# Kernel tuning notes

Measured on AMD Instinct MI355X. Metric: run time of the kernel, lower is better.

## Reference

```python
import jax, jax.numpy as jnp
import numpy as np

N_NODES = 50000
N_EDGES = 1_600_000
F_IN = 128
F_OUT = 8
K_TAPS = 4
AVG_DEG = 32.0


def setup_inputs() -> dict:
    key = jax.random.key(0)
    k1, k2, k3, k4, k5 = jax.random.split(key, 5)
    x = jax.random.normal(k1, (N_NODES, F_IN), dtype=jnp.float32)
    gso_rows = jax.random.randint(k2, (N_EDGES,), 0, N_NODES, dtype=jnp.int32)
    gso_cols = jax.random.randint(k3, (N_EDGES,), 0, N_NODES, dtype=jnp.int32)
    gso_vals = jax.random.uniform(k4, (N_EDGES,), dtype=jnp.float32) / AVG_DEG
    # filterCoeff = randn(outFeat, filter_order) * 0.1 as in torch __init__
    coeff = jax.random.normal(k5, (F_OUT, K_TAPS), dtype=jnp.float32) * 0.1
    return {"x": x, "gso_rows": gso_rows, "gso_cols": gso_cols,
            "gso_vals": gso_vals, "coeff": coeff}


def reference(x, gso_rows, gso_cols, gso_vals, coeff):
    # Faithful to the torch code INCLUDING its carried-over SpMV state:
    # output feature o uses powers S^{1+o(K-1)} .. S^{o(K-1)+K} of x.
    F_out, K = coeff.shape
    N = x.shape[0]
    max_power = F_out * (K - 1) + 1  # highest S power needed

    def spmv(Z):  # S @ Z via edge-list gather + segment_sum scatter
        return jax.ops.segment_sum(gso_vals[:, None] * Z[gso_cols], gso_rows,
                                   num_segments=N)

    def step(Z, _):
        Zn = spmv(Z)
        return Zn, Zn.sum(axis=1)  # sum over in-features done up-front

    # s[p-1, n] = sum_f (S^p x)[n, f], for p = 1..max_power
    _, s = jax.lax.scan(step, x, None, length=max_power)  # (max_power, N)

    # power index (0-based into s) used by output o, tap i: o*(K-1) + i
    idx = jnp.arange(F_out)[:, None] * (K - 1) + jnp.arange(K)[None, :]  # (F_out, K)
    sg = s[idx]  # (F_out, K, N)
    y = jnp.einsum('ok,okn->no', coeff, sg)  # (N, F_out)
    return y
```

## Files before the change

### kernel.cpp

```cpp
#include <hip/hip_runtime.h>
#include <hip/hip_bf16.h>

#define N_NODES 50000
#define NPAD    50176
#define N_EDGES 1600000
#define F_IN    128
#define F_OUT   8
#define K_TAPS  4
#define MAX_POWER 25

#define NBLK    256
#define NTHR    512
#define RPB     196
#define CHUNK   6272
#define NPART   256
#define NTHR_P  512
#define ECAP_G  8192
#define ECAP_L  7168
#define NITER   14
#define CSB     800

typedef int v4i __attribute__((ext_vector_type(4)));

__device__ inline int wave_incl_scan(int v, int lane) {
    #pragma unroll
    for (int off = 1; off < 64; off <<= 1) {
        int t = __shfl_up(v, off, 64);
        if (lane >= off) v += t;
    }
    return v;
}

__device__ inline void st_coh_i(int* p, int v) {
    __hip_atomic_store(p, v, __ATOMIC_RELAXED, __HIP_MEMORY_SCOPE_AGENT);
}
__device__ inline void st_coh_i4(v4i* p, v4i v) {
    asm volatile("global_store_dwordx4 %0, %1, off sc0 sc1"
                 :: "v"(p), "v"(v) : "memory");
}
__device__ inline v4i ld_coh_i4(const v4i* p) {
    v4i v;
    asm volatile("global_load_dwordx4 %0, %1, off sc0 sc1\n\t"
                 "s_waitcnt vmcnt(0)"
                 : "=&v"(v) : "v"(p) : "memory");
    return v;
}

__global__ void rowsum_kernel(const float* __restrict__ x,
                              float* __restrict__ u, int n_nodes) {
    int tid = threadIdx.x;
    int lane = tid & 63;
    int wid = tid >> 6;
    int half = lane >> 5;
    int l = lane & 31;
    int node = blockIdx.x * 8 + wid * 2 + half;
    if (node >= n_nodes) return;
    float4 v = ((const float4*)(x + (size_t)node * F_IN))[l];
    float s = v.x + v.y + v.z + v.w;
    #pragma unroll
    for (int off = 16; off > 0; off >>= 1)
        s += __shfl_down(s, off, 32);
    if (l == 0) u[node] = s;
}

__global__ void partition_kernel(const int* __restrict__ rows,
                                 const int* __restrict__ cols,
                                 const float* __restrict__ vals,
                                 int* __restrict__ gcnt,
                                 int2* __restrict__ edges, int n_edges) {
    __shared__ int lhist[NBLK];
    __shared__ int lcur[NBLK];
    __shared__ int lbase[NBLK];
    __shared__ int2 stage[CHUNK];
    __shared__ unsigned char sbkt[CHUNK];
    __shared__ int wsum[4];
    int tid = threadIdx.x;
    int base = blockIdx.x * CHUNK;
    int cend = min(base + CHUNK, n_edges);

    if (tid < NBLK) lhist[tid] = 0;
    __syncthreads();
    for (int i = base + tid; i < cend; i += NTHR_P)
        atomicAdd(&lhist[rows[i] / RPB], 1);
    __syncthreads();

    int lane = tid & 63, wid = tid >> 6;
    int h = 0, incl = 0;
    if (tid < NBLK) {
        h = lhist[tid];
        incl = wave_incl_scan(h, lane);
        if (lane == 63) wsum[wid] = incl;
    }
    __syncthreads();
    if (tid < NBLK) {
        int woff = 0;
        for (int w = 0; w < wid; ++w) woff += wsum[w];
        int excl = woff + incl - h;
        lcur[tid] = excl;
        if (h) {
            int g = atomicAdd(&gcnt[tid], h);
            lbase[tid] = tid * ECAP_G + g - excl;
        }
    }
    __syncthreads();

    for (int i = base + tid; i < cend; i += NTHR_P) {
        int r = rows[i], c = cols[i];
        float v = vals[i];
        int b = r / RPB;
        int pos = atomicAdd(&lcur[b], 1);
        stage[pos] = make_int2(((r - b * RPB) << 16) | c, __float_as_int(v));
        sbkt[pos] = (unsigned char)b;
    }
    __syncthreads();

    int cn = cend - base;
    for (int i = tid; i < cn; i += NTHR_P) {
        int b = sbkt[i];
        int o = lbase[b] + i;
        if (o - b * ECAP_G < ECAP_G)
            edges[o] = stage[i];
    }
}

__global__ __launch_bounds__(NTHR, 1)
void chain_kernel(const int* __restrict__ gcnt,
                  const int2* __restrict__ edges,
                  const float* __restrict__ coeff,
                  const float* __restrict__ u,
                  float* __restrict__ s,
                  float* __restrict__ y,
                  int* __restrict__ flags,
                  int n_nodes) {
    __shared__ int2  esort[ECAP_L];
    __shared__ int   chist[CSB];
    __shared__ int   ccur[CSB];
    __shared__ int   wsum8[8];
    __shared__ __align__(16) float acc[RPB];
    __shared__ float yacc[RPB * F_OUT];
    __shared__ float lcoeff[F_OUT * K_TAPS];

    int tid = threadIdx.x;
    int b = blockIdx.x;

    if (tid < RPB) acc[tid] = 0.f;
    for (int j = tid; j < RPB * F_OUT; j += NTHR) yacc[j] = 0.f;
    if (tid < F_OUT * K_TAPS) lcoeff[tid] = coeff[tid];

    int cnt = min(gcnt[b], ECAP_G);
    const int2* eb = edges + (size_t)b * ECAP_G;

    for (int i = tid; i < CSB; i += NTHR) chist[i] = 0;
    __syncthreads();
    if (cnt <= ECAP_L) {
        for (int i = tid; i < cnt; i += NTHR) {
            int2 e = eb[i];
            atomicAdd(&chist[(e.x & 0xFFFF) >> 6], 1);
        }
        __syncthreads();
        int lane = tid & 63, wid = tid >> 6;
        int b0 = 2 * tid;
        int h0 = (b0 < CSB) ? chist[b0] : 0;
        int h1 = (b0 + 1 < CSB) ? chist[b0 + 1] : 0;
        int ps = h0 + h1;
        int incl = wave_incl_scan(ps, lane);
        if (lane == 63) wsum8[wid] = incl;
        __syncthreads();
        int woff = 0;
        for (int w = 0; w < wid; ++w) woff += wsum8[w];
        int ex = woff + incl - ps;
        if (b0 < CSB) ccur[b0] = ex;
        if (b0 + 1 < CSB) ccur[b0 + 1] = ex + h0;
        __syncthreads();
        for (int i = tid; i < cnt; i += NTHR) {
            int2 e = eb[i];
            int pos = atomicAdd(&ccur[(e.x & 0xFFFF) >> 6], 1);
            esort[pos] = e;
        }
        __syncthreads();
    } else {
        int cl = min(cnt, ECAP_L);
        for (int i = tid; i < cl; i += NTHR) esort[i] = eb[i];
        __syncthreads();
    }

    int   ecol[NITER];
    int   erow[NITER];
    float eval[NITER];
    int cntl = min(cnt, ECAP_L);
    #pragma unroll
    for (int j = 0; j < NITER; ++j) {
        int idx = tid + j * NTHR;
        int2 e = (idx < cntl) ? esort[idx] : make_int2(0, 0);
        ecol[j] = e.x & 0xFFFF;
        erow[j] = e.x >> 16;
        eval[j] = __int_as_float(e.y);
    }

    for (int p = 0; p < MAX_POWER; ++p) {
        const float* __restrict__ src = (p == 0) ? u : s + (size_t)(p - 1) * NPAD;
        float* dst = s + (size_t)p * NPAD;

        float v[NITER];
        #pragma unroll
        for (int j = 0; j < NITER; ++j) v[j] = src[ecol[j]];
        #pragma unroll
        for (int j = 0; j < NITER; ++j)
            if (tid + j * NTHR < cntl)
                atomicAdd(&acc[erow[j]], eval[j] * v[j]);
        for (int k = ECAP_L + tid; k < cnt; k += NTHR) {
            int2 ev = eb[k];
            atomicAdd(&acc[ev.x >> 16], __int_as_float(ev.y) * src[ev.x & 0xFFFF]);
        }
        __syncthreads();

        float val = (tid < RPB) ? acc[tid] : 0.f;
        bool last = (p == MAX_POWER - 1);

        if (!last && tid < RPB / 4) {
            v4i av = ((const v4i*)acc)[tid];
            st_coh_i4(((v4i*)(dst + (size_t)b * RPB)) + tid, av);
        }

        if (tid < RPB) {
            #pragma unroll
            for (int o = 0; o < F_OUT; ++o) {
                int k = p - (K_TAPS - 1) * o;
                if (k >= 0 && k < K_TAPS)
                    yacc[tid * F_OUT + o] += lcoeff[o * K_TAPS + k] * val;
            }
        }

        if (!last) {
            if (tid == 0) {
                asm volatile("s_waitcnt vmcnt(0)" ::: "memory");
                st_coh_i(&flags[b], p + 1);
            }
            __syncthreads();
            if (tid < RPB) acc[tid] = 0.f;
            if (tid < NBLK / 4) {
                const v4i* fp = ((const v4i*)flags) + tid;
                int target = p + 1;
                while (true) {
                    v4i f = ld_coh_i4(fp);
                    int m = min(min(f[0], f[1]), min(f[2], f[3]));
                    if (__all(m >= target)) break;
                    __builtin_amdgcn_s_sleep(1);
                }
            }
            __syncthreads();
        }
    }

    __syncthreads();
    for (int j = tid; j < RPB * F_OUT; j += NTHR) {
        int row = b * RPB + (j >> 3);
        if (row < n_nodes) y[(size_t)row * F_OUT + (j & 7)] = yacc[j];
    }
}

extern "C" void kernel_launch(void* const* d_in, const int* in_sizes, int n_in,
                              void* d_out, int out_size, void* d_ws, size_t ws_size,
                              hipStream_t stream) {
    const float* x        = (const float*)d_in[0];
    const int*   gso_rows = (const int*)d_in[1];
    const int*   gso_cols = (const int*)d_in[2];
    const float* gso_vals = (const float*)d_in[3];
    const float* coeff    = (const float*)d_in[4];
    float* y = (float*)d_out;

    float* u     = (float*)d_ws;
    float* s     = u + NPAD;
    int2*  edges = (int2*)(s + (size_t)MAX_POWER * NPAD);
    int*   gcnt  = (int*)(edges + (size_t)NBLK * ECAP_G);
    int*   flags = gcnt + NBLK;

    (void)hipMemsetAsync(gcnt, 0, (size_t)(NBLK + NBLK) * sizeof(int), stream);

    partition_kernel<<<NPART, NTHR_P, 0, stream>>>(
        gso_rows, gso_cols, gso_vals, gcnt, edges, N_EDGES);

    rowsum_kernel<<<(N_NODES + 7) / 8, 256, 0, stream>>>(x, u, N_NODES);

    int n_nodes = N_NODES;
    void* args[] = { (void*)&gcnt, (void*)&edges, (void*)&coeff,
                     (void*)&u, (void*)&s, (void*)&y, (void*)&flags,
                     (void*)&n_nodes };
    (void)hipLaunchCooperativeKernel((void*)chain_kernel, dim3(NBLK), dim3(NTHR),
                                     args, 0, stream);
}
```

Before: 475.8 us.

## Replace grid-wide flag barrier with per-element sentinel polling dataflow

Removes the per-power grid barrier built on a flags array. Instead, every power buffer is pre-filled with a NaN sentinel and consumers poll each gathered value until it is no longer the sentinel. The accumulator is double-buffered so the block needs only one __syncthreads per power. The goal is to let blocks proceed as soon as their actual dependencies are ready, at the cost of an extra poison fill and agent-scope atomic loads with retry loops.

```diff
diff --git a/kernel.cpp b/kernel.cpp
--- a/kernel.cpp
+++ b/kernel.cpp
@@ -1,5 +1,4 @@
 #include <hip/hip_runtime.h>
-#include <hip/hip_bf16.h>
 
 #define N_NODES 50000
 #define NPAD    50176
@@ -20,7 +19,7 @@
 #define NITER   14
 #define CSB     800
 
-typedef int v4i __attribute__((ext_vector_type(4)));
+#define SENT_I  (-1)
 
 __device__ inline int wave_incl_scan(int v, int lane) {
     #pragma unroll
@@ -31,23 +30,22 @@
     return v;
 }
 
-__device__ inline void st_coh_i(int* p, int v) {
+__device__ inline float ld_agent_f(const float* p) {
+    return __hip_atomic_load((const float*)p, __ATOMIC_RELAXED, __HIP_MEMORY_SCOPE_AGENT);
+}
+__device__ inline void st_agent_f(float* p, float v) {
     __hip_atomic_store(p, v, __ATOMIC_RELAXED, __HIP_MEMORY_SCOPE_AGENT);
 }
-__device__ inline void st_coh_i4(v4i* p, v4i v) {
-    asm volatile("global_store_dwordx4 %0, %1, off sc0 sc1"
-                 :: "v"(p), "v"(v) : "memory");
-}
-__device__ inline v4i ld_coh_i4(const v4i* p) {
-    v4i v;
-    asm volatile("global_load_dwordx4 %0, %1, off sc0 sc1\n\t"
-                 "s_waitcnt vmcnt(0)"
-                 : "=&v"(v) : "v"(p) : "memory");
-    return v;
-}
 
 __global__ void rowsum_kernel(const float* __restrict__ x,
-                              float* __restrict__ u, int n_nodes) {
+                              float* __restrict__ u,
+                              int* __restrict__ spoison,
+                              int n_nodes) {
+    int gid = blockIdx.x * 256 + threadIdx.x;
+    const int SP = 24 * NPAD;
+    for (int i = gid; i < SP; i += gridDim.x * 256)
+        spoison[i] = SENT_I;
+
     int tid = threadIdx.x;
     int lane = tid & 63;
     int wid = tid >> 6;
@@ -107,18 +105,18 @@
     for (int i = base + tid; i < cend; i += NTHR_P) {
         int r = rows[i], c = cols[i];
         float v = vals[i];
-        int b = r / RPB;
-        int pos = atomicAdd(&lcur[b], 1);
-        stage[pos] = make_int2(((r - b * RPB) << 16) | c, __float_as_int(v));
-        sbkt[pos] = (unsigned char)b;
+        int bb = r / RPB;
+        int pos = atomicAdd(&lcur[bb], 1);
+        stage[pos] = make_int2(((r - bb * RPB) << 16) | c, __float_as_int(v));
+        sbkt[pos] = (unsigned char)bb;
     }
     __syncthreads();
 
     int cn = cend - base;
     for (int i = tid; i < cn; i += NTHR_P) {
-        int b = sbkt[i];
-        int o = lbase[b] + i;
-        if (o - b * ECAP_G < ECAP_G)
+        int bb = sbkt[i];
+        int o = lbase[bb] + i;
+        if (o - bb * ECAP_G < ECAP_G)
             edges[o] = stage[i];
     }
 }
@@ -130,20 +128,19 @@
                   const float* __restrict__ u,
                   float* __restrict__ s,
                   float* __restrict__ y,
-                  int* __restrict__ flags,
                   int n_nodes) {
     __shared__ int2  esort[ECAP_L];
     __shared__ int   chist[CSB];
     __shared__ int   ccur[CSB];
     __shared__ int   wsum8[8];
-    __shared__ __align__(16) float acc[RPB];
+    __shared__ float acc[2][RPB];
     __shared__ float yacc[RPB * F_OUT];
     __shared__ float lcoeff[F_OUT * K_TAPS];
 
     int tid = threadIdx.x;
     int b = blockIdx.x;
 
-    if (tid < RPB) acc[tid] = 0.f;
+    if (tid < RPB) { acc[0][tid] = 0.f; acc[1][tid] = 0.f; }
     for (int j = tid; j < RPB * F_OUT; j += NTHR) yacc[j] = 0.f;
     if (tid < F_OUT * K_TAPS) lcoeff[tid] = coeff[tid];
 
@@ -188,6 +185,7 @@
     int   erow[NITER];
     float eval[NITER];
     int cntl = min(cnt, ECAP_L);
+    unsigned pend0 = 0;
     #pragma unroll
     for (int j = 0; j < NITER; ++j) {
         int idx = tid + j * NTHR;
@@ -195,61 +193,63 @@
         ecol[j] = e.x & 0xFFFF;
         erow[j] = e.x >> 16;
         eval[j] = __int_as_float(e.y);
-    }
-
+        if (idx < cntl) pend0 |= (1u << j);
+    }
+
+    int cur = 0;
     for (int p = 0; p < MAX_POWER; ++p) {
         const float* __restrict__ src = (p == 0) ? u : s + (size_t)(p - 1) * NPAD;
         float* dst = s + (size_t)p * NPAD;
 
         float v[NITER];
-        #pragma unroll
-        for (int j = 0; j < NITER; ++j) v[j] = src[ecol[j]];
+        if (p == 0) {
+            #pragma unroll
+            for (int j = 0; j < NITER; ++j) v[j] = src[ecol[j]];
+        } else {
+            unsigned pend = pend0;
+            while (pend) {
+                float t[NITER];
+                #pragma unroll
+                for (int j = 0; j < NITER; ++j)
+                    if (pend & (1u << j)) t[j] = ld_agent_f(&src[ecol[j]]);
+                #pragma unroll
+                for (int j = 0; j < NITER; ++j)
+                    if ((pend & (1u << j)) && __float_as_int(t[j]) != SENT_I) {
+                        v[j] = t[j];
+                        pend &= ~(1u << j);
+                    }
+                if (pend) __builtin_amdgcn_s_sleep(2);
+            }
+        }
+
+        float* accc = acc[cur];
         #pragma unroll
         for (int j = 0; j < NITER; ++j)
             if (tid + j * NTHR < cntl)
-                atomicAdd(&acc[erow[j]], eval[j] * v[j]);
+                atomicAdd(&accc[erow[j]], eval[j] * v[j]);
         for (int k = ECAP_L + tid; k < cnt; k += NTHR) {
             int2 ev = eb[k];
-            atomicAdd(&acc[ev.x >> 16], __int_as_float(ev.y) * src[ev.x & 0xFFFF]);
-        }
-        __syncthreads();
-
-        float val = (tid < RPB) ? acc[tid] : 0.f;
+            float sv;
+            if (p == 0) sv = src[ev.x & 0xFFFF];
+            else do { sv = ld_agent_f(&src[ev.x & 0xFFFF]); }
+                 while (__float_as_int(sv) == SENT_I);
+            atomicAdd(&accc[ev.x >> 16], __int_as_float(ev.y) * sv);
+        }
+        __syncthreads();
+
         bool last = (p == MAX_POWER - 1);
-
-        if (!last && tid < RPB / 4) {
-            v4i av = ((const v4i*)acc)[tid];
-            st_coh_i4(((v4i*)(dst + (size_t)b * RPB)) + tid, av);
-        }
-
         if (tid < RPB) {
+            float val = accc[tid];
+            if (!last) st_agent_f(&dst[b * RPB + tid], val);
             #pragma unroll
             for (int o = 0; o < F_OUT; ++o) {
                 int k = p - (K_TAPS - 1) * o;
                 if (k >= 0 && k < K_TAPS)
                     yacc[tid * F_OUT + o] += lcoeff[o * K_TAPS + k] * val;
             }
-        }
-
-        if (!last) {
-            if (tid == 0) {
-                asm volatile("s_waitcnt vmcnt(0)" ::: "memory");
-                st_coh_i(&flags[b], p + 1);
-            }
-            __syncthreads();
-            if (tid < RPB) acc[tid] = 0.f;
-            if (tid < NBLK / 4) {
-                const v4i* fp = ((const v4i*)flags) + tid;
-                int target = p + 1;
-                while (true) {
-                    v4i f = ld_coh_i4(fp);
-                    int m = min(min(f[0], f[1]), min(f[2], f[3]));
-                    if (__all(m >= target)) break;
-                    __builtin_amdgcn_s_sleep(1);
-                }
-            }
-            __syncthreads();
-        }
+            accc[tid] = 0.f;
+        }
+        cur ^= 1;
     }
 
     __syncthreads();
@@ -273,19 +273,17 @@
     float* s     = u + NPAD;
     int2*  edges = (int2*)(s + (size_t)MAX_POWER * NPAD);
     int*   gcnt  = (int*)(edges + (size_t)NBLK * ECAP_G);
-    int*   flags = gcnt + NBLK;
-
-    (void)hipMemsetAsync(gcnt, 0, (size_t)(NBLK + NBLK) * sizeof(int), stream);
+
+    (void)hipMemsetAsync(gcnt, 0, (size_t)NBLK * sizeof(int), stream);
 
     partition_kernel<<<NPART, NTHR_P, 0, stream>>>(
         gso_rows, gso_cols, gso_vals, gcnt, edges, N_EDGES);
 
-    rowsum_kernel<<<(N_NODES + 7) / 8, 256, 0, stream>>>(x, u, N_NODES);
+    rowsum_kernel<<<(N_NODES + 7) / 8, 256, 0, stream>>>(x, u, (int*)s, N_NODES);
 
     int n_nodes = N_NODES;
     void* args[] = { (void*)&gcnt, (void*)&edges, (void*)&coeff,
-                     (void*)&u, (void*)&s, (void*)&y, (void*)&flags,
-                     (void*)&n_nodes };
+                     (void*)&u, (void*)&s, (void*)&y, (void*)&n_nodes };
     (void)hipLaunchCooperativeKernel((void*)chain_kernel, dim3(NBLK), dim3(NTHR),
                                      args, 0, stream);
 }
```

After: 411.1 us. -13.6%, faster.
